# Performance work log

Measured on AMD Instinct MI355X. Metric: run time of the kernel, lower is better.

Reference implementation:

```python
import jax, jax.numpy as jnp
import numpy as np

N_TOKEN = 50000
D_EMBED = 512
D_PROJ = 1024
CUTOFFS = [10000, 30000, 50000]  # cutoffs + [n_token]
N_CLUSTERS = len(CUTOFFS) - 1    # 2


def setup_inputs() -> dict:
    key = jax.random.key(0)
    ks = jax.random.split(key, 8)
    s = 0.02
    return {
        "hidden": jax.random.normal(ks[0], (4096, D_PROJ), jnp.float32),
        "target": jax.random.randint(ks[1], (4096,), 0, N_TOKEN, jnp.int64),
        # div_val == 1: one big output embedding, sliced per cluster
        "weight": jax.random.normal(ks[2], (N_TOKEN, D_EMBED), jnp.float32) * s,
        "bias": jnp.zeros((N_TOKEN,), jnp.float32),
        "cluster_weight": jax.random.normal(ks[3], (N_CLUSTERS, D_EMBED), jnp.float32) * s,
        "cluster_bias": jnp.zeros((N_CLUSTERS,), jnp.float32),
        # one [d_proj, d_embed] projection per cluster (head + 2 tails)
        "projs": jax.random.normal(ks[4], (N_CLUSTERS + 1, D_PROJ, D_EMBED), jnp.float32) * s,
    }


def _adaptive_logprob(hidden, target, weight, bias, cluster_weight, cluster_bias, projs):
    c0 = CUTOFFS[0]
    n = hidden.shape[0]
    # head: first-cluster vocab + one logit per tail cluster
    head_w = jnp.concatenate([weight[:c0], cluster_weight], axis=0)      # [c0+K, d_embed]
    head_b = jnp.concatenate([bias[:c0], cluster_bias], axis=0)          # [c0+K]
    h0 = hidden @ projs[0]                                               # [N, d_embed]
    head_lp = jax.nn.log_softmax(h0 @ head_w.T + head_b, axis=-1)        # [N, c0+K]

    # tokens in head cluster
    head_idx = jnp.clip(target, 0, c0 - 1)
    lp = jnp.take_along_axis(head_lp, head_idx[:, None], axis=1)[:, 0]
    out = jnp.where(target < c0, lp, 0.0)

    # tail clusters
    for i in range(1, N_CLUSTERS + 1):
        l, r = CUTOFFS[i - 1], CUTOFFS[i]
        hi = hidden @ projs[i]                                           # [N, d_embed]
        tail_lp = jax.nn.log_softmax(hi @ weight[l:r].T + bias[l:r], axis=-1)  # [N, r-l]
        t_idx = jnp.clip(target - l, 0, r - l - 1)
        tlp = jnp.take_along_axis(tail_lp, t_idx[:, None], axis=1)[:, 0]
        lp_i = head_lp[:, c0 + i - 1] + tlp
        out = jnp.where((target >= l) & (target < r), lp_i, out)

    return -out  # nll per token, [N]


def reference(hidden, target, weight, bias, cluster_weight, cluster_bias, projs):
    tgt_len = target.shape[0]
    nll = _adaptive_logprob(hidden[-tgt_len:], target, weight, bias,
                            cluster_weight, cluster_bias, projs)
    return nll.reshape(tgt_len, -1)  # [N, 1], matches loss.view(tgt_len, -1)
```

## Files before the change

kernel.cpp:

```cpp
#include <hip/hip_runtime.h>
#include <math.h>

#define NT 4096
#define DP 1024
#define DE 512
#define C0 10000
#define CUT1 30000
#define TAILV 20000
#define WROWS 50112

typedef unsigned short ushort_t;
typedef short bf8 __attribute__((ext_vector_type(8)));
typedef float f4 __attribute__((ext_vector_type(4)));

__device__ __forceinline__ ushort_t f2b(float f) {
    union { float f; unsigned int u; } v; v.f = f;
    unsigned int r = v.u + 0x7FFFu + ((v.u >> 16) & 1u);
    return (ushort_t)(r >> 16);
}
__device__ __forceinline__ float b2f(ushort_t u) {
    union { unsigned int u; float f; } v; v.u = ((unsigned int)u) << 16; return v.f;
}

__device__ __forceinline__ void gld16(const void* g, void* l) {
    __builtin_amdgcn_global_load_lds(
        (const __attribute__((address_space(1))) unsigned int*)g,
        (__attribute__((address_space(3))) unsigned int*)l, 16, 0, 0);
}

__device__ __forceinline__ int xcd_swz(int wgid, int nwg) {
    int q = nwg >> 3, r = nwg & 7;
    int xcd = wgid & 7, idx = wgid >> 3;
    int base = (xcd < r) ? xcd * (q + 1) : r * (q + 1) + (xcd - r) * q;
    return base + idx;
}

__global__ void cluster_kernel(const int* __restrict__ target,
                               int* __restrict__ cnt, int* __restrict__ list) {
    int t = blockIdx.x * blockDim.x + threadIdx.x;
    if (t >= NT) return;
    int tgt = target[t];
    int c = (tgt < C0) ? 0 : (tgt < CUT1 ? 1 : 2);
    if (c > 0) {
        int pos = atomicAdd(&cnt[c - 1], 1);
        list[(c - 1) * NT + pos] = t;
    }
}

__global__ __launch_bounds__(256)
void cast_pad(const float* __restrict__ in, ushort_t* __restrict__ out,
              int total4, int valid) {
    int i = blockIdx.x * 256 + threadIdx.x;
    if (i >= total4) return;
    int base = i * 4;
    unsigned long long p = 0ull;
    if (base < valid) {
        float4 v = *reinterpret_cast<const float4*>(in + base);
        p = (unsigned long long)f2b(v.x)
          | ((unsigned long long)f2b(v.y) << 16)
          | ((unsigned long long)f2b(v.z) << 32)
          | ((unsigned long long)f2b(v.w) << 48);
    }
    *reinterpret_cast<unsigned long long*>(out + base) = p;
}

__global__ __launch_bounds__(256)
void transpose_cast(const float* __restrict__ projs, ushort_t* __restrict__ out) {
    const int cblk = blockIdx.z;
    const int n0 = blockIdx.x * 32;
    const int k0 = blockIdx.y * 32;
    __shared__ float tile[32][33];
    const int tx = threadIdx.x & 31, ty = threadIdx.x >> 5;
    const float* src = projs + (size_t)cblk * DP * DE;
    #pragma unroll
    for (int j = 0; j < 4; ++j)
        tile[ty + j * 8][tx] = src[(size_t)(k0 + ty + j * 8) * DE + n0 + tx];
    __syncthreads();
    ushort_t* dst = out + (size_t)cblk * DE * DP;
    #pragma unroll
    for (int j = 0; j < 4; ++j)
        dst[(size_t)(n0 + ty + j * 8) * DP + k0 + tx] = f2b(tile[tx][ty + j * 8]);
}

template<int MODE>
__global__ __launch_bounds__(256, 4)
void gemm_bt(const ushort_t* __restrict__ Ab, const ushort_t* __restrict__ Bb,
             ushort_t* __restrict__ Cout, float* __restrict__ Sout,
             const float* __restrict__ bias,
             const int* __restrict__ cnt, const int* __restrict__ list,
             int K, int validN)
{
    const int tid = threadIdx.x;
    const int lane = tid & 63;
    const int wave = tid >> 6;
    const int wr = wave >> 1, wc = wave & 1;

    const int logical = xcd_swz(blockIdx.x, gridDim.x);
    const int bm = (logical & 31) * 128;
    const int bn = (logical >> 5) * 128;

    int n = 0;
    if (MODE == 0) {
        Bb += (size_t)blockIdx.z * DE * DP;
        Cout += (size_t)blockIdx.z * (size_t)NT * DE;
    }
    if (MODE == 2) {
        const int tail = blockIdx.z;
        n = cnt[tail];
        if (bm >= n) return;
        Ab += (size_t)(1 + tail) * NT * DE;
        Bb += (size_t)(C0 + tail * TAILV) * DE;
        bias += C0 + tail * TAILV;
        list += tail * NT;
    }

    __shared__ __align__(16) unsigned char lds[32768];
    unsigned char* As = lds;
    unsigned char* Bs = lds + 16384;

    const int kswz = (lane & 7) ^ ((lane >> 3) & 7);
    const int kbase = kswz * 8;
    const int srow = wave * 8 + (lane >> 3);

    size_t arow[4], brow[4];
    #pragma unroll
    for (int s = 0; s < 4; ++s) {
        int lr = s * 32 + srow;
        int ga;
        if (MODE == 2) {
            int gr = bm + lr;
            ga = (gr < n) ? list[gr] : 0;
        } else ga = bm + lr;
        arow[s] = (size_t)ga * K;
        brow[s] = (size_t)(bn + lr) * K;
    }

    f4 acc[4][4];
    const f4 zero = {0.f, 0.f, 0.f, 0.f};
    #pragma unroll
    for (int i = 0; i < 4; ++i)
        #pragma unroll
        for (int j = 0; j < 4; ++j) acc[i][j] = zero;

    for (int kt = 0; kt < K; kt += 64) {
        if (kt) __syncthreads();
        #pragma unroll
        for (int s = 0; s < 4; ++s) {
            gld16(Ab + arow[s] + kt + kbase, As + s * 4096 + wave * 1024);
            gld16(Bb + brow[s] + kt + kbase, Bs + s * 4096 + wave * 1024);
        }
        __syncthreads();
        #pragma unroll
        for (int kh = 0; kh < 2; ++kh) {
            bf8 af[4], bv[4];
            #pragma unroll
            for (int i = 0; i < 4; ++i) {
                const int R = wr * 64 + i * 16 + (lane & 15);
                af[i] = *reinterpret_cast<const bf8*>(
                    As + R * 128 + (((kh * 4 + (lane >> 4)) ^ (R & 7)) << 4));
                const int Rb = wc * 64 + i * 16 + (lane & 15);
                bv[i] = *reinterpret_cast<const bf8*>(
                    Bs + Rb * 128 + (((kh * 4 + (lane >> 4)) ^ (Rb & 7)) << 4));
            }
            #pragma unroll
            for (int i = 0; i < 4; ++i)
                #pragma unroll
                for (int j = 0; j < 4; ++j)
                    acc[i][j] = __builtin_amdgcn_mfma_f32_16x16x32_bf16(
                        af[i], bv[j], acc[i][j], 0, 0, 0);
        }
    }

    if (MODE == 0) {
        #pragma unroll
        for (int i = 0; i < 4; ++i) {
            const int row = bm + wr * 64 + i * 16 + ((lane >> 4) << 2);
            #pragma unroll
            for (int j = 0; j < 4; ++j) {
                const int col = bn + wc * 64 + j * 16 + (lane & 15);
                #pragma unroll
                for (int r = 0; r < 4; ++r)
                    Cout[(size_t)(row + r) * DE + col] = f2b(acc[i][j][r]);
            }
        }
    } else {
        float rs[4][4];
        #pragma unroll
        for (int i = 0; i < 4; ++i)
            #pragma unroll
            for (int r = 0; r < 4; ++r) {
                float s = 0.f;
                #pragma unroll
                for (int j = 0; j < 4; ++j) {
                    const int col = bn + wc * 64 + j * 16 + (lane & 15);
                    if (col < validN) s += __expf(acc[i][j][r] + bias[col]);
                }
                rs[i][r] = s;
            }
        #pragma unroll
        for (int m = 1; m < 16; m <<= 1)
            #pragma unroll
            for (int i = 0; i < 4; ++i)
                #pragma unroll
                for (int r = 0; r < 4; ++r)
                    rs[i][r] += __shfl_xor(rs[i][r], m);
        if ((lane & 15) == 0) {
            const int rb = (lane >> 4) << 2;
            #pragma unroll
            for (int i = 0; i < 4; ++i)
                #pragma unroll
                for (int r = 0; r < 4; ++r) {
                    const int rloc = wr * 64 + i * 16 + rb + r;
                    if (MODE == 1) {
                        atomicAdd(&Sout[bm + rloc], rs[i][r]);
                    } else {
                        int gm = bm + rloc;
                        if (gm < n) atomicAdd(&Sout[list[gm]], rs[i][r]);
                    }
                }
        }
    }
}

__global__ __launch_bounds__(64)
void finalize_kernel(const ushort_t* __restrict__ Hb, const int* __restrict__ target,
                     const float* __restrict__ weight, const float* __restrict__ bias,
                     const float* __restrict__ cw, const float* __restrict__ cb,
                     const float* __restrict__ S_head, const float* __restrict__ S_tail,
                     float* __restrict__ out)
{
    const int t = blockIdx.x, lane = threadIdx.x;
    const int tgt = target[t];
    const int c = (tgt < C0) ? 0 : (tgt < CUT1 ? 1 : 2);
    const int e = lane * 8;

    union { uint4 u; ushort_t s[8]; } h0;
    h0.u = *reinterpret_cast<const uint4*>(Hb + (size_t)t * DE + e);
    float hv[8];
    #pragma unroll
    for (int k = 0; k < 8; ++k) hv[k] = b2f(h0.s[k]);

    float c1 = 0.f, c2 = 0.f;
    #pragma unroll
    for (int k = 0; k < 8; ++k) {
        c1 += hv[k] * cw[e + k];
        c2 += hv[k] * cw[DE + e + k];
    }

    const ushort_t* hs = (c == 0) ? (Hb + (size_t)t * DE)
                                  : (Hb + ((size_t)c * NT + (size_t)t) * DE);
    union { uint4 u; ushort_t s[8]; } hc;
    hc.u = *reinterpret_cast<const uint4*>(hs + e);
    const float* wt = weight + (size_t)tgt * DE;
    float dt = 0.f;
    #pragma unroll
    for (int k = 0; k < 8; ++k) dt += b2f(hc.s[k]) * wt[e + k];

    #pragma unroll
    for (int m = 32; m; m >>= 1) {
        c1 += __shfl_xor(c1, m);
        c2 += __shfl_xor(c2, m);
        dt += __shfl_xor(dt, m);
    }
    if (lane == 0) {
        c1 += cb[0]; c2 += cb[1];
        const float S = S_head[t] + __expf(c1) + __expf(c2);
        const float lsh = logf(S);
        float res;
        if (c == 0) {
            res = lsh - (dt + bias[tgt]);
        } else {
            const float cl = (c == 1) ? c1 : c2;
            res = (lsh - cl) + (logf(S_tail[t]) - (dt + bias[tgt]));
        }
        out[t] = res;
    }
}

extern "C" void kernel_launch(void* const* d_in, const int* in_sizes, int n_in,
                              void* d_out, int out_size, void* d_ws, size_t ws_size,
                              hipStream_t stream) {
    const float* hidden = (const float*)d_in[0];
    const int*   target = (const int*)d_in[1];
    const float* weight = (const float*)d_in[2];
    const float* bias   = (const float*)d_in[3];
    const float* cw     = (const float*)d_in[4];
    const float* cb     = (const float*)d_in[5];
    const float* projs  = (const float*)d_in[6];
    float* out = (float*)d_out;

    char* w = (char*)d_ws;
    ushort_t* Hb      = (ushort_t*)w;  w += (size_t)3 * NT * DE * 2;
    ushort_t* hiddenb = (ushort_t*)w;  w += (size_t)NT * DP * 2;
    ushort_t* Wb      = (ushort_t*)w;  w += (size_t)WROWS * DE * 2;
    ushort_t* projsTb = (ushort_t*)w;  w += (size_t)3 * DE * DP * 2;
    float* S_head = (float*)w;         w += NT * 4;
    float* S_tail = (float*)w;         w += NT * 4;
    int* cnt      = (int*)w;           w += 32;
    int* list     = (int*)w;           w += 2 * NT * 4;

    hipMemsetAsync(S_head, 0, NT * 4 * 2 + 32, stream);
    cluster_kernel<<<NT / 256, 256, 0, stream>>>(target, cnt, list);
    cast_pad<<<(NT * DP / 4 + 255) / 256, 256, 0, stream>>>(
        hidden, hiddenb, NT * DP / 4, NT * DP);
    cast_pad<<<(WROWS * DE / 4 + 255) / 256, 256, 0, stream>>>(
        weight, Wb, WROWS * DE / 4, 50000 * DE);
    transpose_cast<<<dim3(DE / 32, DP / 32, 3), 256, 0, stream>>>(projs, projsTb);

    gemm_bt<0><<<dim3(32 * 4, 1, 3), 256, 0, stream>>>(
        hiddenb, projsTb, Hb, nullptr, nullptr, nullptr, nullptr, DP, DE);
    gemm_bt<1><<<dim3(32 * 79, 1, 1), 256, 0, stream>>>(
        Hb, Wb, nullptr, S_head, bias, nullptr, nullptr, DE, C0);
    gemm_bt<2><<<dim3(32 * 157, 1, 2), 256, 0, stream>>>(
        Hb, Wb, nullptr, S_tail, bias, cnt, list, DE, TAILV);
    finalize_kernel<<<NT, 64, 0, stream>>>(
        Hb, target, weight, bias, cw, cb, S_head, S_tail, out);
}
```

Measured before the change: 358.8 us.

## Replace row-sum atomics with per-block partial buffers and a reduce kernel

The GEMM epilogues no longer atomically add row exp-sums into S_head/S_tail. Each block now reduces its two column-wave halves in LDS and writes one partial per row into a per-column-block buffer. A new reduce kernel sums those partials and scatters the tail sums through the cluster list. This removes contended global atomics at the cost of extra workspace, an extra launch and two block barriers.

New measurement: 298.8 us. 16.7% less time.

```diff
diff --git a/kernel.cpp b/kernel.cpp
--- a/kernel.cpp
+++ b/kernel.cpp
@@ -8,6 +8,8 @@
 #define CUT1 30000
 #define TAILV 20000
 #define WROWS 50112
+#define NBH 79
+#define NBT 157
 
 typedef unsigned short ushort_t;
 typedef short bf8 __attribute__((ext_vector_type(8)));
@@ -98,6 +100,7 @@
     const int logical = xcd_swz(blockIdx.x, gridDim.x);
     const int bm = (logical & 31) * 128;
     const int bn = (logical >> 5) * 128;
+    const int nb = logical >> 5;
 
     int n = 0;
     if (MODE == 0) {
@@ -112,6 +115,7 @@
         Bb += (size_t)(C0 + tail * TAILV) * DE;
         bias += C0 + tail * TAILV;
         list += tail * NT;
+        Sout += (size_t)tail * NBT * NT;
     }
 
     __shared__ __align__(16) unsigned char lds[32768];
@@ -204,21 +208,42 @@
                 #pragma unroll
                 for (int r = 0; r < 4; ++r)
                     rs[i][r] += __shfl_xor(rs[i][r], m);
+        float* ps = (float*)lds;
+        __syncthreads();
         if ((lane & 15) == 0) {
             const int rb = (lane >> 4) << 2;
             #pragma unroll
             for (int i = 0; i < 4; ++i)
                 #pragma unroll
-                for (int r = 0; r < 4; ++r) {
-                    const int rloc = wr * 64 + i * 16 + rb + r;
-                    if (MODE == 1) {
-                        atomicAdd(&Sout[bm + rloc], rs[i][r]);
-                    } else {
-                        int gm = bm + rloc;
-                        if (gm < n) atomicAdd(&Sout[list[gm]], rs[i][r]);
-                    }
-                }
-        }
+                for (int r = 0; r < 4; ++r)
+                    ps[wc * 128 + wr * 64 + i * 16 + rb + r] = rs[i][r];
+        }
+        __syncthreads();
+        if (tid < 128) {
+            float v = ps[tid] + ps[128 + tid];
+            Sout[(size_t)nb * NT + bm + tid] = v;
+        }
+    }
+}
+
+__global__ __launch_bounds__(256)
+void reduce_kernel(const float* __restrict__ Ph, const float* __restrict__ Pt,
+                   const int* __restrict__ cnt, const int* __restrict__ list,
+                   float* __restrict__ S_head, float* __restrict__ S_tail) {
+    const int z = blockIdx.y;
+    const int t = blockIdx.x * 256 + threadIdx.x;
+    if (z == 0) {
+        if (t >= NT) return;
+        float s = 0.f;
+        for (int nb = 0; nb < NBH; ++nb) s += Ph[(size_t)nb * NT + t];
+        S_head[t] = s;
+    } else {
+        const int tail = z - 1;
+        if (t >= cnt[tail]) return;
+        const float* P = Pt + (size_t)tail * NBT * NT;
+        float s = 0.f;
+        for (int nb = 0; nb < NBT; ++nb) s += P[(size_t)nb * NT + t];
+        S_tail[list[tail * NT + t]] = s;
     }
 }
 
@@ -298,8 +323,10 @@
     float* S_tail = (float*)w;         w += NT * 4;
     int* cnt      = (int*)w;           w += 32;
     int* list     = (int*)w;           w += 2 * NT * 4;
-
-    hipMemsetAsync(S_head, 0, NT * 4 * 2 + 32, stream);
+    float* Ph     = (float*)w;         w += (size_t)NBH * NT * 4;
+    float* Pt     = (float*)w;         w += (size_t)2 * NBT * NT * 4;
+
+    hipMemsetAsync(cnt, 0, 32, stream);
     cluster_kernel<<<NT / 256, 256, 0, stream>>>(target, cnt, list);
     cast_pad<<<(NT * DP / 4 + 255) / 256, 256, 0, stream>>>(
         hidden, hiddenb, NT * DP / 4, NT * DP);
@@ -309,10 +336,12 @@
 
     gemm_bt<0><<<dim3(32 * 4, 1, 3), 256, 0, stream>>>(
         hiddenb, projsTb, Hb, nullptr, nullptr, nullptr, nullptr, DP, DE);
-    gemm_bt<1><<<dim3(32 * 79, 1, 1), 256, 0, stream>>>(
-        Hb, Wb, nullptr, S_head, bias, nullptr, nullptr, DE, C0);
-    gemm_bt<2><<<dim3(32 * 157, 1, 2), 256, 0, stream>>>(
-        Hb, Wb, nullptr, S_tail, bias, cnt, list, DE, TAILV);
+    gemm_bt<1><<<dim3(32 * NBH, 1, 1), 256, 0, stream>>>(
+        Hb, Wb, nullptr, Ph, bias, nullptr, nullptr, DE, C0);
+    gemm_bt<2><<<dim3(32 * NBT, 1, 2), 256, 0, stream>>>(
+        Hb, Wb, nullptr, Pt, bias, cnt, list, DE, TAILV);
+    reduce_kernel<<<dim3(NT / 256, 3), 256, 0, stream>>>(
+        Ph, Pt, cnt, list, S_head, S_tail);
     finalize_kernel<<<NT, 64, 0, stream>>>(
         Hb, target, weight, bias, cw, cb, S_head, S_tail, out);
 }
```
